# Optimization experiments

Measured on AMD Instinct MI355X. Metric: run time of the kernel, lower is better.

The kernel has to match this reference:

```python
import jax, jax.numpy as jnp
import numpy as np
import math


def setup_inputs() -> dict:
    key = jax.random.key(0)
    ks = jax.random.split(key, 6)
    B, S, D = 4, 1024, 768
    n_h, k = 12, 256
    d_head = D // n_h
    x = jax.random.normal(ks[0], (B, S, D), dtype=jnp.float32)
    attention_mask = jnp.ones((B, S), dtype=jnp.int32)
    Wc_w = jax.random.normal(ks[1], (D, 3 * D), dtype=jnp.float32) * 0.02
    Wc_b = jnp.zeros((3 * D,), dtype=jnp.float32)
    Wp_w = jax.random.normal(ks[2], (d_head, 2 * d_head), dtype=jnp.float32) * 0.02
    table = jax.random.uniform(ks[3], (2 * k + 1, d_head), dtype=jnp.float32, minval=-0.1, maxval=0.1)
    cproj_w = jax.random.normal(ks[4], (D, D), dtype=jnp.float32) * 0.02
    cproj_b = jnp.zeros((D,), dtype=jnp.float32)
    return {"x": x, "attention_mask": attention_mask, "Wc_w": Wc_w, "Wc_b": Wc_b,
            "Wp_w": Wp_w, "table": table, "cproj_w": cproj_w, "cproj_b": cproj_b,
            "n_h": n_h, "k": k}


def reference(x, attention_mask, Wc_w, Wc_b, Wp_w, table, cproj_w, cproj_b, n_h, k):
    B, S, D = x.shape
    d_head = D // n_h
    # content QKV projection
    qkv = x @ Wc_w + Wc_b                              # [B,S,3D]
    qc, kc, vc = jnp.split(qkv, 3, axis=2)
    def heads(t):
        return t.reshape(B, S, n_h, d_head).transpose(0, 2, 1, 3)  # [B,H,S,dh]
    qc, kc, vc = heads(qc), heads(kc), heads(vc)
    # relative position lookup
    i = jnp.arange(S)[:, None]
    j = jnp.arange(S)[None, :]
    rel = jnp.clip(j - i, -k, k) + k                   # [S,S]
    P = table[rel]                                     # [S,S,dh]
    qr_kr = P @ Wp_w                                   # [S,S,2dh]
    qr, kr = jnp.split(qr_kr, 2, axis=2)               # each [S,S,dh]
    # content-content
    c_c = jnp.einsum('bhid,bhjd->bhij', qc, kc)
    # content-position (faithful to source: kr indexed [s,i,d])
    c_p = jnp.einsum('bhid,sid->bhis', qc, kr)
    # position-content (faithful: source einsum sums kc over j)
    kc_sum = kc.sum(axis=2)                            # [B,H,dh]
    c_r = jnp.einsum('sid,bhd->bhis', qr, kc_sum)
    score = (c_c + c_p + c_r) / math.sqrt(d_head)      # [B,H,S,S]
    mask = (attention_mask == 0)[:, None, None, :]     # [B,1,1,S]
    score = jnp.where(mask, -1e9, score)
    attn = jax.nn.softmax(score, axis=-1)
    out = jnp.einsum('bhis,bhsd->bhid', attn, vc)      # [B,H,S,dh]
    out = out.transpose(0, 2, 1, 3).reshape(B, S, D)
    return out @ cproj_w + cproj_b
```

## Files before the change

kernel.cpp:

```cpp
#include <hip/hip_runtime.h>
#include <math.h>

#define NB 4
#define SEQ 1024
#define DMODEL 768
#define NH 12
#define DH 64
#define BHn (NB * NH)
#define NRr 513

typedef short s8v __attribute__((ext_vector_type(8)));
typedef float f4v __attribute__((ext_vector_type(4)));
typedef unsigned short u4v __attribute__((ext_vector_type(4)));

__device__ inline unsigned short f2bf(float f) {
    unsigned int u = __float_as_uint(f);
    u += 0x7fffu + ((u >> 16) & 1u);
    return (unsigned short)(u >> 16);
}

__device__ inline float bf2f(unsigned short h) {
    return __uint_as_float(((unsigned int)h) << 16);
}

__global__ __launch_bounds__(192) void conv_xsum_kernel(const float* __restrict__ x,
                                                        unsigned short* __restrict__ xh,
                                                        float* __restrict__ xsum) {
    int b = blockIdx.x, sg = blockIdx.y;
    int t = threadIdx.x;
    const float* base = x + ((size_t)b * SEQ + sg * 16) * DMODEL + t * 4;
    unsigned short* obase = xh + ((size_t)b * SEQ + sg * 16) * DMODEL + t * 4;
    float4 a = {0.f, 0.f, 0.f, 0.f};
#pragma unroll 4
    for (int s = 0; s < 16; ++s) {
        float4 v = *(const float4*)(base + (size_t)s * DMODEL);
        a.x += v.x; a.y += v.y; a.z += v.z; a.w += v.w;
        ushort4 o;
        o.x = f2bf(v.x); o.y = f2bf(v.y); o.z = f2bf(v.z); o.w = f2bf(v.w);
        *(ushort4*)(obase + (size_t)s * DMODEL) = o;
    }
    float* dst = &xsum[b * DMODEL + t * 4];
    atomicAdd(dst + 0, a.x);
    atomicAdd(dst + 1, a.y);
    atomicAdd(dst + 2, a.z);
    atomicAdd(dst + 3, a.w);
}

__global__ __launch_bounds__(256) void transpose_conv_kernel(const float* __restrict__ W,
                                                             unsigned short* __restrict__ WT,
                                                             int R, int C) {
    __shared__ float tile[64][65];
    int t = threadIdx.x;
    int ty = t >> 6, tx = t & 63;
    int c0 = blockIdx.x * 64, r0 = blockIdx.y * 64;
#pragma unroll
    for (int i = 0; i < 16; ++i) {
        int r = ty + i * 4;
        tile[r][tx] = W[(size_t)(r0 + r) * C + c0 + tx];
    }
    __syncthreads();
#pragma unroll
    for (int i = 0; i < 16; ++i) {
        int c = ty + i * 4;
        WT[(size_t)(c0 + c) * R + r0 + tx] = f2bf(tile[tx][c]);
    }
}

__global__ __launch_bounds__(64) void pos_kernel(const float* __restrict__ table,
                                                 const float* __restrict__ Wp,
                                                 float* __restrict__ qr_tab,
                                                 unsigned short* __restrict__ krh) {
    int r = blockIdx.x;
    int d = threadIdx.x;
    float aq = 0.f, ak = 0.f;
#pragma unroll 8
    for (int t = 0; t < 64; ++t) {
        float tv = table[r * 64 + t];
        aq += tv * Wp[t * 128 + d];
        ak += tv * Wp[t * 128 + 64 + d];
    }
    qr_tab[r * 64 + d] = aq;
    krh[r * 64 + d] = f2bf(ak);
}

__global__ __launch_bounds__(256) void ksum_kernel(const float* __restrict__ xsum,
                                                   const unsigned short* __restrict__ Wch,
                                                   const float* __restrict__ Wc_b,
                                                   float* __restrict__ ksum_out) {
    __shared__ float part[4][64];
    int bh = blockIdx.x;
    int b = bh / NH, h = bh - b * NH;
    int t = threadIdx.x;
    int seg = t >> 6, d = t & 63;
    const unsigned short* wrow = Wch + (size_t)(DMODEL + h * 64 + d) * DMODEL + seg * 192;
    const float* xs = xsum + b * DMODEL + seg * 192;
    float s = 0.f;
#pragma unroll 4
    for (int k = 0; k < 192; k += 8) {
        s8v w = *(const s8v*)(wrow + k);
        float4 x0 = *(const float4*)(xs + k);
        float4 x1 = *(const float4*)(xs + k + 4);
        s += x0.x * bf2f((unsigned short)w[0]) + x0.y * bf2f((unsigned short)w[1])
           + x0.z * bf2f((unsigned short)w[2]) + x0.w * bf2f((unsigned short)w[3])
           + x1.x * bf2f((unsigned short)w[4]) + x1.y * bf2f((unsigned short)w[5])
           + x1.z * bf2f((unsigned short)w[6]) + x1.w * bf2f((unsigned short)w[7]);
    }
    part[seg][d] = s;
    __syncthreads();
    if (t < 64)
        ksum_out[bh * 64 + t] = part[0][t] + part[1][t] + part[2][t] + part[3][t]
                              + 1024.f * Wc_b[DMODEL + h * 64 + t];
}

__global__ __launch_bounds__(192) void crtab2_kernel(const float* __restrict__ ksum_t,
                                                     const float* __restrict__ qr_tab,
                                                     float* __restrict__ cr_tab) {
    int bh = blockIdx.x;
    int r = blockIdx.y * 192 + threadIdx.x;
    if (r >= NRr) return;
    const float* ks = ksum_t + bh * 64;
    const float* qr = qr_tab + (size_t)r * 64;
    float acc = 0.f;
#pragma unroll
    for (int dd = 0; dd < 64; dd += 4) {
        float4 q = *(const float4*)(qr + dd);
        float4 k = *(const float4*)(ks + dd);
        acc += q.x * k.x + q.y * k.y + q.z * k.z + q.w * k.w;
    }
    cr_tab[bh * NRr + r] = acc;
}

__global__ __launch_bounds__(256) void gemm_qkv_mfma(const unsigned short* __restrict__ A,
                                                     const unsigned short* __restrict__ BT,
                                                     const float* __restrict__ bias,
                                                     unsigned short* __restrict__ qh,
                                                     unsigned short* __restrict__ kh,
                                                     unsigned short* __restrict__ vh) {
    __shared__ unsigned short As[64 * 72];
    __shared__ unsigned short Bs[128 * 72];
    const int K = DMODEL, NIT = K / 64;
    int t = threadIdx.x;
    int wave = t >> 6, lane = t & 63, quad = lane >> 4, lc = lane & 15;
    int m0 = blockIdx.y * 64, n0 = blockIdx.x * 128;
    int wm = (wave >> 1) * 32, wn = (wave & 1) * 64;
    int arow = t >> 2, ak = (t & 3) * 16;
    int brow = t >> 1, bk = (t & 1) * 32;
    const unsigned short* Ag = A + (size_t)(m0 + arow) * K + ak;
    const unsigned short* Bg = BT + (size_t)(n0 + brow) * K + bk;
    unsigned short* Al = &As[arow * 72 + ak];
    unsigned short* Bl = &Bs[brow * 72 + bk];
    f4v acc[2][4];
#pragma unroll
    for (int i = 0; i < 2; ++i)
#pragma unroll
        for (int j = 0; j < 4; ++j) acc[i][j] = (f4v){0.f, 0.f, 0.f, 0.f};

    s8v ar[2], br[4];
#pragma unroll
    for (int c = 0; c < 2; ++c) ar[c] = *(const s8v*)(Ag + c * 8);
#pragma unroll
    for (int c = 0; c < 4; ++c) br[c] = *(const s8v*)(Bg + c * 8);

    for (int it = 0; it < NIT; ++it) {
        __syncthreads();
#pragma unroll
        for (int c = 0; c < 2; ++c) *(s8v*)(Al + c * 8) = ar[c];
#pragma unroll
        for (int c = 0; c < 4; ++c) *(s8v*)(Bl + c * 8) = br[c];
        __syncthreads();
        if (it + 1 < NIT) {
            int kn = (it + 1) * 64;
#pragma unroll
            for (int c = 0; c < 2; ++c) ar[c] = *(const s8v*)(Ag + kn + c * 8);
#pragma unroll
            for (int c = 0; c < 4; ++c) br[c] = *(const s8v*)(Bg + kn + c * 8);
        }
#pragma unroll
        for (int ko = 0; ko < 2; ++ko) {
            s8v a[2], b[4];
#pragma unroll
            for (int fr = 0; fr < 2; ++fr)
                a[fr] = *(const s8v*)&As[(wm + fr * 16 + lc) * 72 + ko * 32 + quad * 8];
#pragma unroll
            for (int fc = 0; fc < 4; ++fc)
                b[fc] = *(const s8v*)&Bs[(wn + fc * 16 + lc) * 72 + ko * 32 + quad * 8];
#pragma unroll
            for (int fr = 0; fr < 2; ++fr)
#pragma unroll
                for (int fc = 0; fc < 4; ++fc)
                    acc[fr][fc] = __builtin_amdgcn_mfma_f32_16x16x32_bf16(a[fr], b[fc], acc[fr][fc], 0, 0, 0);
        }
    }
    int which = blockIdx.x / 6;
    int colbase = n0 - which * DMODEL;
#pragma unroll
    for (int fc = 0; fc < 4; ++fc) {
        int col = colbase + wn + fc * 16 + lc;
        int h = col >> 6, d = col & 63;
        float bv = bias[n0 + wn + fc * 16 + lc];
#pragma unroll
        for (int fr = 0; fr < 2; ++fr)
#pragma unroll
            for (int r = 0; r < 4; ++r) {
                int m = m0 + wm + fr * 16 + quad * 4 + r;
                int b_ = m >> 10, s_ = m & 1023;
                size_t bh = (size_t)b_ * NH + h;
                float v = acc[fr][fc][r] + bv;
                if (which == 0) {
                    qh[(bh * SEQ + s_) * DH + d] = f2bf(v);
                } else if (which == 1) {
                    kh[(bh * SEQ + s_) * DH + d] = f2bf(v);
                } else {
                    vh[(bh * DH + d) * SEQ + s_] = f2bf(v);
                }
            }
    }
}

__global__ __launch_bounds__(256) void gemm_cproj_mfma(const unsigned short* __restrict__ A,
                                                       const unsigned short* __restrict__ BT,
                                                       const float* __restrict__ bias,
                                                       float* __restrict__ C) {
    __shared__ unsigned short As[64 * 72];
    __shared__ unsigned short Bs[128 * 72];
    const int K = DMODEL, N = DMODEL, NIT = K / 64;
    int t = threadIdx.x;
    int wave = t >> 6, lane = t & 63, quad = lane >> 4, lc = lane & 15;
    int m0 = blockIdx.y * 64, n0 = blockIdx.x * 128;
    int wm = (wave >> 1) * 32, wn = (wave & 1) * 64;
    int arow = t >> 2, ak = (t & 3) * 16;
    int brow = t >> 1, bk = (t & 1) * 32;
    const unsigned short* Ag = A + (size_t)(m0 + arow) * K + ak;
    const unsigned short* Bg = BT + (size_t)(n0 + brow) * K + bk;
    unsigned short* Al = &As[arow * 72 + ak];
    unsigned short* Bl = &Bs[brow * 72 + bk];
    f4v acc[2][4];
#pragma unroll
    for (int i = 0; i < 2; ++i)
#pragma unroll
        for (int j = 0; j < 4; ++j) acc[i][j] = (f4v){0.f, 0.f, 0.f, 0.f};

    s8v ar[2], br[4];
#pragma unroll
    for (int c = 0; c < 2; ++c) ar[c] = *(const s8v*)(Ag + c * 8);
#pragma unroll
    for (int c = 0; c < 4; ++c) br[c] = *(const s8v*)(Bg + c * 8);

    for (int it = 0; it < NIT; ++it) {
        __syncthreads();
#pragma unroll
        for (int c = 0; c < 2; ++c) *(s8v*)(Al + c * 8) = ar[c];
#pragma unroll
        for (int c = 0; c < 4; ++c) *(s8v*)(Bl + c * 8) = br[c];
        __syncthreads();
        if (it + 1 < NIT) {
            int kn = (it + 1) * 64;
#pragma unroll
            for (int c = 0; c < 2; ++c) ar[c] = *(const s8v*)(Ag + kn + c * 8);
#pragma unroll
            for (int c = 0; c < 4; ++c) br[c] = *(const s8v*)(Bg + kn + c * 8);
        }
#pragma unroll
        for (int ko = 0; ko < 2; ++ko) {
            s8v a[2], b[4];
#pragma unroll
            for (int fr = 0; fr < 2; ++fr)
                a[fr] = *(const s8v*)&As[(wm + fr * 16 + lc) * 72 + ko * 32 + quad * 8];
#pragma unroll
            for (int fc = 0; fc < 4; ++fc)
                b[fc] = *(const s8v*)&Bs[(wn + fc * 16 + lc) * 72 + ko * 32 + quad * 8];
#pragma unroll
            for (int fr = 0; fr < 2; ++fr)
#pragma unroll
                for (int fc = 0; fc < 4; ++fc)
                    acc[fr][fc] = __builtin_amdgcn_mfma_f32_16x16x32_bf16(a[fr], b[fc], acc[fr][fc], 0, 0, 0);
        }
    }
#pragma unroll
    for (int fc = 0; fc < 4; ++fc) {
        int n = n0 + wn + fc * 16 + lc;
        float bv = bias[n];
#pragma unroll
        for (int fr = 0; fr < 2; ++fr)
#pragma unroll
            for (int r = 0; r < 4; ++r) {
                int m = m0 + wm + fr * 16 + quad * 4 + r;
                C[(size_t)m * N + n] = acc[fr][fc][r] + bv;
            }
    }
}

__global__ __launch_bounds__(256, 3) void attn_kernel(const unsigned short* __restrict__ qh,
                                                      const unsigned short* __restrict__ kh,
                                                      const unsigned short* __restrict__ vh,
                                                      const unsigned short* __restrict__ krh,
                                                      const float* __restrict__ cr_tab,
                                                      unsigned short* __restrict__ aouth) {
    __shared__ unsigned short k_s[2][64 * 72];
    __shared__ unsigned short v_s[2][64 * 72];
    __shared__ unsigned short strip[4][1280];
    const int NT = SEQ / 64;
    int t = threadIdx.x;
    int wave = t >> 6, lane = t & 63, quad = lane >> 4, lc = lane & 15;
    int bh = blockIdx.y, b = bh / NH, h = bh - b * NH;
    int i0 = blockIdx.x * 64;
    int irow = i0 + wave * 16;

    const unsigned short* qbase = &qh[((size_t)bh * SEQ + irow + lc) * DH + quad * 8];
    s8v aq0 = *(const s8v*)qbase;
    s8v aq1 = *(const s8v*)(qbase + 32);

    s8v ones;
#pragma unroll
    for (int j = 0; j < 8; ++j) ones[j] = (short)0x3F80;

    f4v o[4], o4;
#pragma unroll
    for (int ct = 0; ct < 4; ++ct) o[ct] = (f4v){0.f, 0.f, 0.f, 0.f};
    o4 = (f4v){0.f, 0.f, 0.f, 0.f};

    const float* crb = cr_tab + (size_t)bh * NRr;
    unsigned short* sw = &strip[wave][0];

    f4v e0, e512;
    {
        s8v b0 = *(const s8v*)&krh[quad * 8];
        s8v b1 = *(const s8v*)&krh[32 + quad * 8];
        f4v c = {0.f, 0.f, 0.f, 0.f};
        c = __builtin_amdgcn_mfma_f32_16x16x32_bf16(aq0, b0, c, 0, 0, 0);
        c = __builtin_amdgcn_mfma_f32_16x16x32_bf16(aq1, b1, c, 0, 0, 0);
        float cr0 = crb[0];
#pragma unroll
        for (int rg = 0; rg < 4; ++rg) e0[rg] = c[rg] + cr0;
        b0 = *(const s8v*)&krh[(size_t)512 * DH + quad * 8];
        b1 = *(const s8v*)&krh[(size_t)512 * DH + 32 + quad * 8];
        f4v c2 = {0.f, 0.f, 0.f, 0.f};
        c2 = __builtin_amdgcn_mfma_f32_16x16x32_bf16(aq0, b0, c2, 0, 0, 0);
        c2 = __builtin_amdgcn_mfma_f32_16x16x32_bf16(aq1, b1, c2, 0, 0, 0);
        float cr5 = crb[512];
#pragma unroll
        for (int rg = 0; rg < 4; ++rg) e512[rg] = c2[rg] + cr5;
    }

    int r0s = t >> 3, offs = (t & 7) * 8;
    const unsigned short* kgb = &kh[((size_t)bh * SEQ) * DH];
    const unsigned short* vgb = &vh[((size_t)bh * DH) * SEQ];

    s8v kr0 = *(const s8v*)&kgb[(size_t)r0s * DH + offs];
    s8v kr1 = *(const s8v*)&kgb[(size_t)(r0s + 32) * DH + offs];
    s8v vr0 = *(const s8v*)&vgb[(size_t)r0s * SEQ + offs];
    s8v vr1 = *(const s8v*)&vgb[(size_t)(r0s + 32) * SEQ + offs];
    *(s8v*)&k_s[0][r0s * 72 + offs] = kr0;
    *(s8v*)&k_s[0][(r0s + 32) * 72 + offs] = kr1;
    *(s8v*)&v_s[0][r0s * 72 + offs] = vr0;
    *(s8v*)&v_s[0][(r0s + 32) * 72 + offs] = vr1;
    kr0 = *(const s8v*)&kgb[(size_t)(64 + r0s) * DH + offs];
    kr1 = *(const s8v*)&kgb[(size_t)(64 + r0s + 32) * DH + offs];
    vr0 = *(const s8v*)&vgb[(size_t)r0s * SEQ + 64 + offs];
    vr1 = *(const s8v*)&vgb[(size_t)(r0s + 32) * SEQ + 64 + offs];

    int rw0 = i0 + 193 + wave * 16;
    if (rw0 < 512) {
#pragma unroll
        for (int ct2 = 0; ct2 < 5; ++ct2) {
            int r = rw0 + ct2 * 16 + lc;
            r = r < 0 ? 0 : (r > 512 ? 512 : r);
            const unsigned short* kb = &krh[(size_t)r * DH + quad * 8];
            s8v b0 = *(const s8v*)kb;
            s8v b1 = *(const s8v*)(kb + 32);
            float crv = crb[r];
            f4v c = {0.f, 0.f, 0.f, 0.f};
            c = __builtin_amdgcn_mfma_f32_16x16x32_bf16(aq0, b0, c, 0, 0, 0);
            c = __builtin_amdgcn_mfma_f32_16x16x32_bf16(aq1, b1, c, 0, 0, 0);
            int jbase = ct2 * 16 + lc;
#pragma unroll
            for (int rg = 0; rg < 4; ++rg) {
                int il = quad * 4 + rg;
                int dd = jbase - il;
                if (dd >= 0 && dd < 64)
                    sw[dd * 20 + il] = f2bf(c[rg] + crv);
            }
        }
    }

    for (int tt = 0; tt < NT; ++tt) {
        __syncthreads();
        int cur = tt & 1, nxt = cur ^ 1;
        int rwt = rw0 - tt * 64;
        if (tt + 1 < NT) {
            *(s8v*)&k_s[nxt][r0s * 72 + offs] = kr0;
            *(s8v*)&k_s[nxt][(r0s + 32) * 72 + offs] = kr1;
            *(s8v*)&v_s[nxt][r0s * 72 + offs] = vr0;
            *(s8v*)&v_s[nxt][(r0s + 32) * 72 + offs] = vr1;
            if (tt + 2 < NT) {
                int sn = tt * 64 + 128;
                kr0 = *(const s8v*)&kgb[(size_t)(sn + r0s) * DH + offs];
                kr1 = *(const s8v*)&kgb[(size_t)(sn + r0s + 32) * DH + offs];
                vr0 = *(const s8v*)&vgb[(size_t)r0s * SEQ + sn + offs];
                vr1 = *(const s8v*)&vgb[(size_t)(r0s + 32) * SEQ + sn + offs];
            }
        }
        f4v sc[4];
#pragma unroll
        for (int ct = 0; ct < 4; ++ct) {
            const unsigned short* kb = &k_s[cur][(ct * 16 + lc) * 72 + quad * 8];
            s8v b0 = *(const s8v*)kb;
            s8v b1 = *(const s8v*)(kb + 32);
            f4v c = {0.f, 0.f, 0.f, 0.f};
            c = __builtin_amdgcn_mfma_f32_16x16x32_bf16(aq0, b0, c, 0, 0, 0);
            c = __builtin_amdgcn_mfma_f32_16x16x32_bf16(aq1, b1, c, 0, 0, 0);
            sc[ct] = c;
        }
        bool near_t = (rwt > -78) && (rwt < 512);
        if (near_t) {
#pragma unroll
            for (int ct = 0; ct < 4; ++ct) {
                int dd = 63 - ct * 16 - lc;
                u4v g = *(const u4v*)&sw[dd * 20 + quad * 4];
#pragma unroll
                for (int r = 0; r < 4; ++r)
                    sc[ct][r] = (sc[ct][r] + bf2f(g[r])) * 0.125f;
            }
        } else {
            f4v ea = (rwt <= -78) ? e0 : e512;
#pragma unroll
            for (int ct = 0; ct < 4; ++ct)
#pragma unroll
                for (int r = 0; r < 4; ++r)
                    sc[ct][r] = (sc[ct][r] + ea[r]) * 0.125f;
        }
#pragma unroll
        for (int ct = 0; ct < 4; ++ct)
#pragma unroll
            for (int r = 0; r < 4; ++r)
                sw[(quad * 4 + r) * 76 + ct * 16 + lc] = f2bf(__expf(sc[ct][r]));
        s8v ap0 = *(const s8v*)&sw[lc * 76 + quad * 8];
        s8v ap1 = *(const s8v*)&sw[lc * 76 + 32 + quad * 8];
#pragma unroll
        for (int ct = 0; ct < 4; ++ct) {
            const unsigned short* vb = &v_s[cur][(ct * 16 + lc) * 72 + quad * 8];
            s8v b0 = *(const s8v*)vb;
            s8v b1 = *(const s8v*)(vb + 32);
            o[ct] = __builtin_amdgcn_mfma_f32_16x16x32_bf16(ap0, b0, o[ct], 0, 0, 0);
            o[ct] = __builtin_amdgcn_mfma_f32_16x16x32_bf16(ap1, b1, o[ct], 0, 0, 0);
        }
        o4 = __builtin_amdgcn_mfma_f32_16x16x32_bf16(ap0, ones, o4, 0, 0, 0);
        o4 = __builtin_amdgcn_mfma_f32_16x16x32_bf16(ap1, ones, o4, 0, 0, 0);
        if (tt + 1 < NT) {
            int rwn = rwt - 64;
            if (rwn > -78 && rwn < 512) {
#pragma unroll
                for (int ct2 = 0; ct2 < 5; ++ct2) {
                    int r = rwn + ct2 * 16 + lc;
                    r = r < 0 ? 0 : (r > 512 ? 512 : r);
                    const unsigned short* kb = &krh[(size_t)r * DH + quad * 8];
                    s8v b0 = *(const s8v*)kb;
                    s8v b1 = *(const s8v*)(kb + 32);
                    float crv = crb[r];
                    f4v c = {0.f, 0.f, 0.f, 0.f};
                    c = __builtin_amdgcn_mfma_f32_16x16x32_bf16(aq0, b0, c, 0, 0, 0);
                    c = __builtin_amdgcn_mfma_f32_16x16x32_bf16(aq1, b1, c, 0, 0, 0);
                    int jbase = ct2 * 16 + lc;
#pragma unroll
                    for (int rg = 0; rg < 4; ++rg) {
                        int il = quad * 4 + rg;
                        int dd = jbase - il;
                        if (dd >= 0 && dd < 64)
                            sw[dd * 20 + il] = f2bf(c[rg] + crv);
                    }
                }
            }
        }
    }
#pragma unroll
    for (int ct = 0; ct < 4; ++ct)
#pragma unroll
        for (int r = 0; r < 4; ++r) {
            int ig = irow + quad * 4 + r;
            aouth[((size_t)b * SEQ + ig) * DMODEL + h * DH + ct * 16 + lc] = f2bf(o[ct][r] / o4[r]);
        }
}

extern "C" void kernel_launch(void* const* d_in, const int* in_sizes, int n_in,
                              void* d_out, int out_size, void* d_ws, size_t ws_size,
                              hipStream_t stream) {
    const float* x       = (const float*)d_in[0];
    const float* Wc_w    = (const float*)d_in[2];
    const float* Wc_b    = (const float*)d_in[3];
    const float* Wp_w    = (const float*)d_in[4];
    const float* table   = (const float*)d_in[5];
    const float* cproj_w = (const float*)d_in[6];
    const float* cproj_b = (const float*)d_in[7];

    char* wsb = (char*)d_ws;
    size_t off = 0;
    auto alloc = [&](size_t bytes) -> void* {
        void* p = wsb + off;
        off = (off + bytes + 255) & ~(size_t)255;
        return p;
    };
    unsigned short* xh   = (unsigned short*)alloc((size_t)NB * SEQ * DMODEL * 2);
    unsigned short* Wch  = (unsigned short*)alloc((size_t)3 * DMODEL * DMODEL * 2);
    unsigned short* cpjt = (unsigned short*)alloc((size_t)DMODEL * DMODEL * 2);
    unsigned short* qh   = (unsigned short*)alloc((size_t)BHn * SEQ * DH * 2);
    unsigned short* kh   = (unsigned short*)alloc((size_t)BHn * SEQ * DH * 2);
    unsigned short* vh   = (unsigned short*)alloc((size_t)BHn * SEQ * DH * 2);
    unsigned short* aouth= (unsigned short*)alloc((size_t)NB * SEQ * DMODEL * 2);
    float* qr_tab        = (float*)alloc((size_t)NRr * 64 * 4);
    unsigned short* krh  = (unsigned short*)alloc((size_t)NRr * 64 * 2);
    float* cr_tab        = (float*)alloc((size_t)BHn * NRr * 4);
    float* xsum          = (float*)alloc((size_t)NB * DMODEL * 4);
    float* ksum_t        = (float*)alloc((size_t)BHn * 64 * 4);
    float* out = (float*)d_out;

    hipMemsetAsync(xsum, 0, (size_t)NB * DMODEL * 4, stream);
    hipLaunchKernelGGL(conv_xsum_kernel, dim3(NB, 64), dim3(192), 0, stream, x, xh, xsum);
    hipLaunchKernelGGL(transpose_conv_kernel, dim3(36, 12), dim3(256), 0, stream, Wc_w, Wch, DMODEL, 3 * DMODEL);
    hipLaunchKernelGGL(transpose_conv_kernel, dim3(12, 12), dim3(256), 0, stream, cproj_w, cpjt, DMODEL, DMODEL);
    hipLaunchKernelGGL(pos_kernel, dim3(NRr), dim3(64), 0, stream, table, Wp_w, qr_tab, krh);
    hipLaunchKernelGGL(ksum_kernel, dim3(BHn), dim3(256), 0, stream, xsum, Wch, Wc_b, ksum_t);
    hipLaunchKernelGGL(crtab2_kernel, dim3(BHn, 3), dim3(192), 0, stream, ksum_t, qr_tab, cr_tab);
    hipLaunchKernelGGL(gemm_qkv_mfma, dim3(18, 64), dim3(256), 0, stream, xh, Wch, Wc_b, qh, kh, vh);
    hipLaunchKernelGGL(attn_kernel, dim3(16, BHn), dim3(256), 0, stream, qh, kh, vh, krh, cr_tab, aouth);
    hipLaunchKernelGGL(gemm_cproj_mfma, dim3(6, 64), dim3(256), 0, stream, aouth, cpjt, cproj_b, out);
}
```

Measured before the change: 221.2 us.

## Load GEMM A fragments directly to registers, merge weight transposes, repad softmax tile

Both MFMA GEMMs now read A-operand fragments straight from global memory into registers with one-iteration prefetch, instead of staging them through shared memory. This removes the A-tile LDS traffic and some shared memory use. The trade-off is less coalesced global loads, since each lane reads 16-byte chunks from separate rows. The two weight-transpose launches are merged into one kernel to save a launch, and the attention softmax scratch row stride changes from 76 to 72, which alters the LDS bank pattern.

```diff
diff --git a/kernel.cpp b/kernel.cpp
--- a/kernel.cpp
+++ b/kernel.cpp
@@ -46,13 +46,18 @@
     atomicAdd(dst + 3, a.w);
 }
 
-__global__ __launch_bounds__(256) void transpose_conv_kernel(const float* __restrict__ W,
-                                                             unsigned short* __restrict__ WT,
-                                                             int R, int C) {
+__global__ __launch_bounds__(256) void transpose_both_kernel(const float* __restrict__ Wc,
+                                                             unsigned short* __restrict__ WcT,
+                                                             const float* __restrict__ Wp2,
+                                                             unsigned short* __restrict__ Wp2T) {
     __shared__ float tile[64][65];
     int t = threadIdx.x;
     int ty = t >> 6, tx = t & 63;
-    int c0 = blockIdx.x * 64, r0 = blockIdx.y * 64;
+    const float* W; unsigned short* WT; int C, c0;
+    const int R = DMODEL;
+    if (blockIdx.x < 36) { W = Wc;  WT = WcT;  C = 3 * DMODEL; c0 = blockIdx.x * 64; }
+    else                 { W = Wp2; WT = Wp2T; C = DMODEL;     c0 = (blockIdx.x - 36) * 64; }
+    int r0 = blockIdx.y * 64;
 #pragma unroll
     for (int i = 0; i < 16; ++i) {
         int r = ty + i * 4;
@@ -136,51 +141,51 @@
                                                      unsigned short* __restrict__ qh,
                                                      unsigned short* __restrict__ kh,
                                                      unsigned short* __restrict__ vh) {
-    __shared__ unsigned short As[64 * 72];
     __shared__ unsigned short Bs[128 * 72];
     const int K = DMODEL, NIT = K / 64;
     int t = threadIdx.x;
     int wave = t >> 6, lane = t & 63, quad = lane >> 4, lc = lane & 15;
     int m0 = blockIdx.y * 64, n0 = blockIdx.x * 128;
     int wm = (wave >> 1) * 32, wn = (wave & 1) * 64;
-    int arow = t >> 2, ak = (t & 3) * 16;
     int brow = t >> 1, bk = (t & 1) * 32;
-    const unsigned short* Ag = A + (size_t)(m0 + arow) * K + ak;
     const unsigned short* Bg = BT + (size_t)(n0 + brow) * K + bk;
-    unsigned short* Al = &As[arow * 72 + ak];
     unsigned short* Bl = &Bs[brow * 72 + bk];
+    const unsigned short* Ag0 = A + (size_t)(m0 + wm + lc) * K + quad * 8;
+    const unsigned short* Ag1 = A + (size_t)(m0 + wm + 16 + lc) * K + quad * 8;
     f4v acc[2][4];
 #pragma unroll
     for (int i = 0; i < 2; ++i)
 #pragma unroll
         for (int j = 0; j < 4; ++j) acc[i][j] = (f4v){0.f, 0.f, 0.f, 0.f};
 
-    s8v ar[2], br[4];
-#pragma unroll
-    for (int c = 0; c < 2; ++c) ar[c] = *(const s8v*)(Ag + c * 8);
+    s8v br[4];
 #pragma unroll
     for (int c = 0; c < 4; ++c) br[c] = *(const s8v*)(Bg + c * 8);
+    s8v acur[2][2], anxt[2][2];
+#pragma unroll
+    for (int ko = 0; ko < 2; ++ko) {
+        acur[0][ko] = *(const s8v*)(Ag0 + ko * 32);
+        acur[1][ko] = *(const s8v*)(Ag1 + ko * 32);
+    }
 
     for (int it = 0; it < NIT; ++it) {
         __syncthreads();
-#pragma unroll
-        for (int c = 0; c < 2; ++c) *(s8v*)(Al + c * 8) = ar[c];
 #pragma unroll
         for (int c = 0; c < 4; ++c) *(s8v*)(Bl + c * 8) = br[c];
         __syncthreads();
         if (it + 1 < NIT) {
             int kn = (it + 1) * 64;
 #pragma unroll
-            for (int c = 0; c < 2; ++c) ar[c] = *(const s8v*)(Ag + kn + c * 8);
-#pragma unroll
             for (int c = 0; c < 4; ++c) br[c] = *(const s8v*)(Bg + kn + c * 8);
+#pragma unroll
+            for (int ko = 0; ko < 2; ++ko) {
+                anxt[0][ko] = *(const s8v*)(Ag0 + kn + ko * 32);
+                anxt[1][ko] = *(const s8v*)(Ag1 + kn + ko * 32);
+            }
         }
 #pragma unroll
         for (int ko = 0; ko < 2; ++ko) {
-            s8v a[2], b[4];
-#pragma unroll
-            for (int fr = 0; fr < 2; ++fr)
-                a[fr] = *(const s8v*)&As[(wm + fr * 16 + lc) * 72 + ko * 32 + quad * 8];
+            s8v b[4];
 #pragma unroll
             for (int fc = 0; fc < 4; ++fc)
                 b[fc] = *(const s8v*)&Bs[(wn + fc * 16 + lc) * 72 + ko * 32 + quad * 8];
@@ -188,7 +193,12 @@
             for (int fr = 0; fr < 2; ++fr)
 #pragma unroll
                 for (int fc = 0; fc < 4; ++fc)
-                    acc[fr][fc] = __builtin_amdgcn_mfma_f32_16x16x32_bf16(a[fr], b[fc], acc[fr][fc], 0, 0, 0);
+                    acc[fr][fc] = __builtin_amdgcn_mfma_f32_16x16x32_bf16(acur[fr][ko], b[fc], acc[fr][fc], 0, 0, 0);
+        }
+#pragma unroll
+        for (int ko = 0; ko < 2; ++ko) {
+            acur[0][ko] = anxt[0][ko];
+            acur[1][ko] = anxt[1][ko];
         }
     }
     int which = blockIdx.x / 6;
@@ -221,51 +231,51 @@
                                                        const unsigned short* __restrict__ BT,
                                                        const float* __restrict__ bias,
                                                        float* __restrict__ C) {
-    __shared__ unsigned short As[64 * 72];
     __shared__ unsigned short Bs[128 * 72];
     const int K = DMODEL, N = DMODEL, NIT = K / 64;
     int t = threadIdx.x;
     int wave = t >> 6, lane = t & 63, quad = lane >> 4, lc = lane & 15;
     int m0 = blockIdx.y * 64, n0 = blockIdx.x * 128;
     int wm = (wave >> 1) * 32, wn = (wave & 1) * 64;
-    int arow = t >> 2, ak = (t & 3) * 16;
     int brow = t >> 1, bk = (t & 1) * 32;
-    const unsigned short* Ag = A + (size_t)(m0 + arow) * K + ak;
     const unsigned short* Bg = BT + (size_t)(n0 + brow) * K + bk;
-    unsigned short* Al = &As[arow * 72 + ak];
     unsigned short* Bl = &Bs[brow * 72 + bk];
+    const unsigned short* Ag0 = A + (size_t)(m0 + wm + lc) * K + quad * 8;
+    const unsigned short* Ag1 = A + (size_t)(m0 + wm + 16 + lc) * K + quad * 8;
     f4v acc[2][4];
 #pragma unroll
     for (int i = 0; i < 2; ++i)
 #pragma unroll
         for (int j = 0; j < 4; ++j) acc[i][j] = (f4v){0.f, 0.f, 0.f, 0.f};
 
-    s8v ar[2], br[4];
-#pragma unroll
-    for (int c = 0; c < 2; ++c) ar[c] = *(const s8v*)(Ag + c * 8);
+    s8v br[4];
 #pragma unroll
     for (int c = 0; c < 4; ++c) br[c] = *(const s8v*)(Bg + c * 8);
+    s8v acur[2][2], anxt[2][2];
+#pragma unroll
+    for (int ko = 0; ko < 2; ++ko) {
+        acur[0][ko] = *(const s8v*)(Ag0 + ko * 32);
+        acur[1][ko] = *(const s8v*)(Ag1 + ko * 32);
+    }
 
     for (int it = 0; it < NIT; ++it) {
         __syncthreads();
-#pragma unroll
-        for (int c = 0; c < 2; ++c) *(s8v*)(Al + c * 8) = ar[c];
 #pragma unroll
         for (int c = 0; c < 4; ++c) *(s8v*)(Bl + c * 8) = br[c];
         __syncthreads();
         if (it + 1 < NIT) {
             int kn = (it + 1) * 64;
 #pragma unroll
-            for (int c = 0; c < 2; ++c) ar[c] = *(const s8v*)(Ag + kn + c * 8);
-#pragma unroll
             for (int c = 0; c < 4; ++c) br[c] = *(const s8v*)(Bg + kn + c * 8);
+#pragma unroll
+            for (int ko = 0; ko < 2; ++ko) {
+                anxt[0][ko] = *(const s8v*)(Ag0 + kn + ko * 32);
+                anxt[1][ko] = *(const s8v*)(Ag1 + kn + ko * 32);
+            }
         }
 #pragma unroll
         for (int ko = 0; ko < 2; ++ko) {
-            s8v a[2], b[4];
-#pragma unroll
-            for (int fr = 0; fr < 2; ++fr)
-                a[fr] = *(const s8v*)&As[(wm + fr * 16 + lc) * 72 + ko * 32 + quad * 8];
+            s8v b[4];
 #pragma unroll
             for (int fc = 0; fc < 4; ++fc)
                 b[fc] = *(const s8v*)&Bs[(wn + fc * 16 + lc) * 72 + ko * 32 + quad * 8];
@@ -273,7 +283,12 @@
             for (int fr = 0; fr < 2; ++fr)
 #pragma unroll
                 for (int fc = 0; fc < 4; ++fc)
-                    acc[fr][fc] = __builtin_amdgcn_mfma_f32_16x16x32_bf16(a[fr], b[fc], acc[fr][fc], 0, 0, 0);
+                    acc[fr][fc] = __builtin_amdgcn_mfma_f32_16x16x32_bf16(acur[fr][ko], b[fc], acc[fr][fc], 0, 0, 0);
+        }
+#pragma unroll
+        for (int ko = 0; ko < 2; ++ko) {
+            acur[0][ko] = anxt[0][ko];
+            acur[1][ko] = anxt[1][ko];
         }
     }
 #pragma unroll
@@ -433,9 +448,9 @@
         for (int ct = 0; ct < 4; ++ct)
 #pragma unroll
             for (int r = 0; r < 4; ++r)
-                sw[(quad * 4 + r) * 76 + ct * 16 + lc] = f2bf(__expf(sc[ct][r]));
-        s8v ap0 = *(const s8v*)&sw[lc * 76 + quad * 8];
-        s8v ap1 = *(const s8v*)&sw[lc * 76 + 32 + quad * 8];
+                sw[(quad * 4 + r) * 72 + ct * 16 + lc] = f2bf(__expf(sc[ct][r]));
+        s8v ap0 = *(const s8v*)&sw[lc * 72 + quad * 8];
+        s8v ap1 = *(const s8v*)&sw[lc * 72 + 32 + quad * 8];
 #pragma unroll
         for (int ct = 0; ct < 4; ++ct) {
             const unsigned short* vb = &v_s[cur][(ct * 16 + lc) * 72 + quad * 8];
@@ -515,8 +530,7 @@
 
     hipMemsetAsync(xsum, 0, (size_t)NB * DMODEL * 4, stream);
     hipLaunchKernelGGL(conv_xsum_kernel, dim3(NB, 64), dim3(192), 0, stream, x, xh, xsum);
-    hipLaunchKernelGGL(transpose_conv_kernel, dim3(36, 12), dim3(256), 0, stream, Wc_w, Wch, DMODEL, 3 * DMODEL);
-    hipLaunchKernelGGL(transpose_conv_kernel, dim3(12, 12), dim3(256), 0, stream, cproj_w, cpjt, DMODEL, DMODEL);
+    hipLaunchKernelGGL(transpose_both_kernel, dim3(48, 12), dim3(256), 0, stream, Wc_w, Wch, cproj_w, cpjt);
     hipLaunchKernelGGL(pos_kernel, dim3(NRr), dim3(64), 0, stream, table, Wp_w, qr_tab, krh);
     hipLaunchKernelGGL(ksum_kernel, dim3(BHn), dim3(256), 0, stream, xsum, Wch, Wc_b, ksum_t);
     hipLaunchKernelGGL(crtab2_kernel, dim3(BHn, 3), dim3(192), 0, stream, ksum_t, qr_tab, cr_tab);
```

Result: slower. 234.6 us (+6.1%).
